# Kernel optimization log

Measured on AMD Instinct MI355X. Metric: run time of the kernel, lower is better.

## Reference

```python
import math
import jax, jax.numpy as jnp
import numpy as np

B = 128          # batch_size (graphs)
SEQ = 128        # max_seq_len (nodes per graph)
D = 128          # input_dim
HID = 64         # enc_hidden_dim
HEADS = 4        # in_head
N = B * SEQ      # total nodes
E = 262144       # edges (avg degree 16)


def _make_pe(seq, d):
    pos = np.arange(seq, dtype=np.float32)[:, None]
    i_even = np.arange(0, d, 2, dtype=np.float32)
    pe = np.zeros((seq, d), dtype=np.float32)
    pe[:, 0::2] = np.sin(pos / 10000.0 ** (2.0 * i_even / d))
    pe[:, 1::2] = np.cos(pos / 10000.0 ** (2.0 * (i_even + 1.0) / d))
    return jnp.asarray(pe)


def setup_inputs() -> dict:
    key = jax.random.key(0)
    ks = jax.random.split(key, 10)
    s = 0.1
    return {
        "x": jax.random.normal(ks[0], (N, D), jnp.float32),
        "edge_index": jax.random.randint(ks[1], (2, E), 0, N),
        "pe": _make_pe(SEQ, D),
        "W1": jax.random.normal(ks[2], (D, HEADS * HID), jnp.float32) * s,
        "a_src1": jax.random.normal(ks[3], (HEADS, HID), jnp.float32) * s,
        "a_dst1": jax.random.normal(ks[4], (HEADS, HID), jnp.float32) * s,
        "b1": jnp.zeros((HEADS * HID,), jnp.float32),
        "W2": jax.random.normal(ks[5], (HEADS * HID, HID), jnp.float32) * s,
        "a_src2": jax.random.normal(ks[6], (1, HID), jnp.float32) * s,
        "a_dst2": jax.random.normal(ks[7], (1, HID), jnp.float32) * s,
        "b2": jnp.zeros((HID,), jnp.float32),
        "batch_size": B,
    }


def _gat_conv(x, src, dst, W, a_src, a_dst, b, heads, ch, concat, n):
    # PyG GATConv (eval mode, self-loops already appended to src/dst).
    h = (x @ W).reshape(n, heads, ch)                      # [N,H,C]
    alpha_src = jnp.einsum("nhc,hc->nh", h, a_src)         # [N,H]
    alpha_dst = jnp.einsum("nhc,hc->nh", h, a_dst)
    e = jax.nn.leaky_relu(alpha_src[src] + alpha_dst[dst], 0.2)  # [E,H]
    m = jax.ops.segment_max(e, dst, num_segments=n)        # segment softmax over dst
    ex = jnp.exp(e - m[dst])
    den = jax.ops.segment_sum(ex, dst, num_segments=n)
    alpha = ex / (den[dst] + 1e-16)                        # [E,H]
    out = jax.ops.segment_sum(h[src] * alpha[:, :, None], dst, num_segments=n)
    out = out.reshape(n, heads * ch) if concat else out.mean(axis=1)
    return out + b


def reference(x, edge_index, pe, W1, a_src1, a_dst1, b1, W2, a_src2, a_dst2, b2, batch_size):
    n = x.shape[0]
    loop = jnp.arange(n)
    src = jnp.concatenate([edge_index[0], loop])           # add self-loops (PyG default)
    dst = jnp.concatenate([edge_index[1], loop])
    # positional encoding (dropout inactive in eval)
    h = x * math.sqrt(x.shape[1]) + jnp.tile(pe, (batch_size, 1))
    h = jax.nn.elu(_gat_conv(h, src, dst, W1, a_src1, a_dst1, b1, HEADS, HID, True, n))
    out = _gat_conv(h, src, dst, W2, a_src2, a_dst2, b2, 1, HID, False, n)
    return out.reshape(batch_size, -1, out.shape[1])
```

## Files before the change

### kernel.cpp

```cpp
#include <hip/hip_runtime.h>
#include <hip/hip_bf16.h>

typedef __hip_bfloat16 bf16;

#define N_NODES 16384
#define D_IN    128
#define HID     64
#define HEADS   4
#define F1      256
#define SEQ     128
#define SLOTS   64

__device__ __forceinline__ float wave_sum(float v) {
    #pragma unroll
    for (int o = 32; o > 0; o >>= 1) v += __shfl_xor(v, o, 64);
    return v;
}
__device__ __forceinline__ float lrelu(float v) { return v > 0.f ? v : 0.2f * v; }
__device__ __forceinline__ float rdlane(float v, int l) {
    return __uint_as_float(__builtin_amdgcn_readlane(__float_as_uint(v), l));
}

#define UNPACK8(u, te, acc)                                          \
    do {                                                             \
        acc[0] += (te) * __uint_as_float((u).x << 16);               \
        acc[1] += (te) * __uint_as_float((u).x & 0xffff0000u);       \
        acc[2] += (te) * __uint_as_float((u).y << 16);               \
        acc[3] += (te) * __uint_as_float((u).y & 0xffff0000u);       \
        acc[4] += (te) * __uint_as_float((u).z << 16);               \
        acc[5] += (te) * __uint_as_float((u).z & 0xffff0000u);       \
        acc[6] += (te) * __uint_as_float((u).w << 16);               \
        acc[7] += (te) * __uint_as_float((u).w & 0xffff0000u);       \
    } while (0)

__global__ __launch_bounds__(256) void k_gemm1z(const float* __restrict__ x,
                                                const float* __restrict__ pe,
                                                const float* __restrict__ W1,
                                                const float* __restrict__ a_src1,
                                                const float* __restrict__ a_dst1,
                                                bf16* __restrict__ h,
                                                float* __restrict__ as1,
                                                float* __restrict__ ad1,
                                                int4* __restrict__ cntv) {
    int tid = threadIdx.x, lane = tid & 63, wv = tid >> 6;
    if (tid < 4) cntv[blockIdx.x * 4 + tid] = make_int4(0, 0, 0, 0);

    int base = blockIdx.x * 16;
    int j4 = lane * 4;
    float2 xr[4];
    #pragma unroll
    for (int i = 0; i < 4; i++) {
        int row = base + wv * 4 + i;
        float2 xa  = *(const float2*)(x  + (size_t)row * 128 + 2 * lane);
        float2 pea = *(const float2*)(pe + (size_t)(row & (SEQ - 1)) * 128 + 2 * lane);
        xr[i].x = xa.x * 11.313708499f + pea.x;
        xr[i].y = xa.y * 11.313708499f + pea.y;
    }
    float acc[4][4] = {};
    const float4* Wv = (const float4*)W1;
    #pragma unroll 4
    for (int k2 = 0; k2 < 64; k2++) {
        float4 w0 = Wv[(size_t)(2 * k2) * 64 + lane];
        float4 w1 = Wv[(size_t)(2 * k2 + 1) * 64 + lane];
        #pragma unroll
        for (int i = 0; i < 4; i++) {
            float a0 = rdlane(xr[i].x, k2);
            float a1 = rdlane(xr[i].y, k2);
            acc[i][0] += a0 * w0.x + a1 * w1.x;
            acc[i][1] += a0 * w0.y + a1 * w1.y;
            acc[i][2] += a0 * w0.z + a1 * w1.z;
            acc[i][3] += a0 * w0.w + a1 * w1.w;
        }
    }
    float4 asv = *(const float4*)(a_src1 + j4);
    float4 adv = *(const float4*)(a_dst1 + j4);
    #pragma unroll
    for (int i = 0; i < 4; i++) {
        int row = base + wv * 4 + i;
        union { bf16 b[4]; ushort4 u; } cv;
        cv.b[0] = __float2bfloat16(acc[i][0]);
        cv.b[1] = __float2bfloat16(acc[i][1]);
        cv.b[2] = __float2bfloat16(acc[i][2]);
        cv.b[3] = __float2bfloat16(acc[i][3]);
        *(ushort4*)(h + (size_t)row * 256 + j4) = cv.u;
        float vs = acc[i][0] * asv.x + acc[i][1] * asv.y + acc[i][2] * asv.z + acc[i][3] * asv.w;
        float vd = acc[i][0] * adv.x + acc[i][1] * adv.y + acc[i][2] * adv.z + acc[i][3] * adv.w;
        #pragma unroll
        for (int o = 1; o < 16; o <<= 1) {
            vs += __shfl_xor(vs, o);
            vd += __shfl_xor(vd, o);
        }
        if ((lane & 15) == 0) {
            as1[row * 4 + (lane >> 4)] = vs;
            ad1[row * 4 + (lane >> 4)] = vd;
        }
    }
}

__global__ __launch_bounds__(256) void k_scatter(const int* __restrict__ ei, int E, int Etot,
                                                 int* __restrict__ cnt,
                                                 int* __restrict__ esrc,
                                                 const float* __restrict__ as1,
                                                 const float* __restrict__ ad1,
                                                 float* __restrict__ et) {
    int e = blockIdx.x * 256 + threadIdx.x;
    if (e >= Etot) return;
    int s, d;
    if (e < E) { s = ei[e]; d = ei[E + e]; }
    else       { s = e - E; d = s; }
    int pos = atomicAdd(&cnt[d], 1);
    if (pos < SLOTS) {
        esrc[d * SLOTS + pos] = s;
        float4 av = *(const float4*)(as1 + (size_t)s * 4);
        float4 bv = *(const float4*)(ad1 + (size_t)d * 4);
        size_t eb = (size_t)d * 4 * SLOTS + pos;
        et[eb + 0 * SLOTS] = __expf(lrelu(av.x + bv.x) - 40.f);
        et[eb + 1 * SLOTS] = __expf(lrelu(av.y + bv.y) - 40.f);
        et[eb + 2 * SLOTS] = __expf(lrelu(av.z + bv.z) - 40.f);
        et[eb + 3 * SLOTS] = __expf(lrelu(av.w + bv.w) - 40.f);
    }
}

__global__ __launch_bounds__(256) void k_agg1_gemm2(
        const int* __restrict__ cnt, const int* __restrict__ esrc,
        const float* __restrict__ et,
        const bf16* __restrict__ h,
        const float* __restrict__ b1,
        const float* __restrict__ W2,
        const float* __restrict__ a_src2, const float* __restrict__ a_dst2,
        bf16* __restrict__ h2, float* __restrict__ as2, float* __restrict__ ad2) {
    __shared__ float hs[8][256];
    __shared__ float part[4][8][64];
    int tid = threadIdx.x, lane = tid & 63, wv = tid >> 6;
    int dbase = blockIdx.x * 8;

    int eg = lane >> 3;
    int cg_ = lane & 7;
    const bf16* hbase = h + (size_t)wv * 64 + cg_ * 8;

    int cv = cnt[dbase + (lane & 7)];

    #pragma unroll 2
    for (int it = 0; it < 8; it++) {
        int d = dbase + it;
        int deg = min(__shfl(cv, it), SLOTS);
        int s = esrc[(size_t)d * SLOTS + lane] & (N_NODES - 1);
        float tv = et[((size_t)d * 4 + wv) * SLOTS + lane];
        float t = (lane < deg) ? tv : 0.f;

        float acc[8] = {0, 0, 0, 0, 0, 0, 0, 0};
        for (int sub = 0; sub < deg; sub += 32) {
            int qn = (min(deg - sub, 32) + 7) >> 3;
            int se0, se1, se2, se3; float te0, te1, te2, te3;
            uint4 u0, u1, u2, u3;
            se0 = __shfl(s, sub + eg);      te0 = __shfl(t, sub + eg);
            u0 = *(const uint4*)(hbase + (size_t)se0 * 256);
            if (qn > 1) {
                se1 = __shfl(s, sub + 8 + eg);  te1 = __shfl(t, sub + 8 + eg);
                u1 = *(const uint4*)(hbase + (size_t)se1 * 256);
            }
            if (qn > 2) {
                se2 = __shfl(s, sub + 16 + eg); te2 = __shfl(t, sub + 16 + eg);
                u2 = *(const uint4*)(hbase + (size_t)se2 * 256);
            }
            if (qn > 3) {
                se3 = __shfl(s, sub + 24 + eg); te3 = __shfl(t, sub + 24 + eg);
                u3 = *(const uint4*)(hbase + (size_t)se3 * 256);
            }
            UNPACK8(u0, te0, acc);
            if (qn > 1) UNPACK8(u1, te1, acc);
            if (qn > 2) UNPACK8(u2, te2, acc);
            if (qn > 3) UNPACK8(u3, te3, acc);
        }
        #pragma unroll
        for (int j = 0; j < 8; j++) {
            acc[j] += __shfl_xor(acc[j], 8);
            acc[j] += __shfl_xor(acc[j], 16);
            acc[j] += __shfl_xor(acc[j], 32);
        }
        float den = wave_sum(t);
        if (lane < 8) {
            float inv = 1.f / den;
            int cbase = wv * 64 + lane * 8;
            float o[8];
            #pragma unroll
            for (int j = 0; j < 8; j++) {
                float v = acc[j] * inv + b1[cbase + j];
                o[j] = v > 0.f ? v : (__expf(v) - 1.f);
            }
            float4* dst = (float4*)&hs[it][cbase];
            dst[0] = make_float4(o[0], o[1], o[2], o[3]);
            dst[1] = make_float4(o[4], o[5], o[6], o[7]);
        }
    }
    __syncthreads();

    {
        float acc2[8] = {0, 0, 0, 0, 0, 0, 0, 0};
        const int k4base = wv * 16;
        for (int kk = 0; kk < 16; kk++) {
            int k4 = k4base + kk;
            const float* wp = W2 + (size_t)k4 * 256 + lane;
            float w0 = wp[0], w1 = wp[64], w2 = wp[128], w3 = wp[192];
            #pragma unroll
            for (int r = 0; r < 8; r++) {
                float4 u = *(const float4*)&hs[r][k4 * 4];
                acc2[r] += u.x * w0 + u.y * w1 + u.z * w2 + u.w * w3;
            }
        }
        #pragma unroll
        for (int r = 0; r < 8; r++) part[wv][r][lane] = acc2[r];
    }
    __syncthreads();
    {
        int r0 = wv * 2, r1 = r0 + 1;
        float a0 = part[0][r0][lane] + part[1][r0][lane] + part[2][r0][lane] + part[3][r0][lane];
        float a1 = part[0][r1][lane] + part[1][r1][lane] + part[2][r1][lane] + part[3][r1][lane];
        float asj = a_src2[lane], adj = a_dst2[lane];
        int n0 = dbase + r0, n1 = dbase + r1;
        h2[(size_t)n0 * 64 + lane] = __float2bfloat16(a0);
        h2[(size_t)n1 * 64 + lane] = __float2bfloat16(a1);
        float va0 = wave_sum(a0 * asj);
        float vd0 = wave_sum(a0 * adj);
        float va1 = wave_sum(a1 * asj);
        float vd1 = wave_sum(a1 * adj);
        if (lane == 0) {
            as2[n0] = va0; ad2[n0] = vd0;
            as2[n1] = va1; ad2[n1] = vd1;
        }
    }
}

__global__ __launch_bounds__(256) void k_agg2(const int* __restrict__ cnt,
                                              const int* __restrict__ esrc,
                                              const bf16* __restrict__ h2,
                                              const float* __restrict__ as2,
                                              const float* __restrict__ ad2,
                                              const float* __restrict__ b2v,
                                              float* __restrict__ out) {
    int tid = threadIdx.x, lane = tid & 63, wv = tid >> 6;
    int d = blockIdx.x * 4 + wv;
    int deg = min(cnt[d], SLOTS);
    float adw = ad2[d];
    int eg = lane >> 3, cg_ = lane & 7;
    const bf16* hbase = h2 + cg_ * 8;

    int s = esrc[(size_t)d * SLOTS + lane] & (N_NODES - 1);
    float ev = as2[s];
    float t = (lane < deg) ? __expf(lrelu(ev + adw) - 40.f) : 0.f;

    float acc[8] = {0, 0, 0, 0, 0, 0, 0, 0};
    for (int sub = 0; sub < deg; sub += 32) {
        int qn = (min(deg - sub, 32) + 7) >> 3;
        int se0, se1, se2, se3; float te0, te1, te2, te3;
        uint4 u0, u1, u2, u3;
        se0 = __shfl(s, sub + eg);      te0 = __shfl(t, sub + eg);
        u0 = *(const uint4*)(hbase + (size_t)se0 * 64);
        if (qn > 1) {
            se1 = __shfl(s, sub + 8 + eg);  te1 = __shfl(t, sub + 8 + eg);
            u1 = *(const uint4*)(hbase + (size_t)se1 * 64);
        }
        if (qn > 2) {
            se2 = __shfl(s, sub + 16 + eg); te2 = __shfl(t, sub + 16 + eg);
            u2 = *(const uint4*)(hbase + (size_t)se2 * 64);
        }
        if (qn > 3) {
            se3 = __shfl(s, sub + 24 + eg); te3 = __shfl(t, sub + 24 + eg);
            u3 = *(const uint4*)(hbase + (size_t)se3 * 64);
        }
        UNPACK8(u0, te0, acc);
        if (qn > 1) UNPACK8(u1, te1, acc);
        if (qn > 2) UNPACK8(u2, te2, acc);
        if (qn > 3) UNPACK8(u3, te3, acc);
    }
    #pragma unroll
    for (int j = 0; j < 8; j++) {
        acc[j] += __shfl_xor(acc[j], 8);
        acc[j] += __shfl_xor(acc[j], 16);
        acc[j] += __shfl_xor(acc[j], 32);
    }
    float den = wave_sum(t);
    if (lane < 8) {
        float inv = 1.f / den;
        int cbase = lane * 8;
        float o[8];
        #pragma unroll
        for (int j = 0; j < 8; j++) o[j] = acc[j] * inv + b2v[cbase + j];
        float4* dst = (float4*)(out + (size_t)d * 64 + cbase);
        dst[0] = make_float4(o[0], o[1], o[2], o[3]);
        dst[1] = make_float4(o[4], o[5], o[6], o[7]);
    }
}

extern "C" void kernel_launch(void* const* d_in, const int* in_sizes, int n_in,
                              void* d_out, int out_size, void* d_ws, size_t ws_size,
                              hipStream_t stream) {
    const float* x    = (const float*)d_in[0];
    const int*   ei   = (const int*)  d_in[1];
    const float* pe   = (const float*)d_in[2];
    const float* W1   = (const float*)d_in[3];
    const float* a_s1 = (const float*)d_in[4];
    const float* a_d1 = (const float*)d_in[5];
    const float* b1   = (const float*)d_in[6];
    const float* W2   = (const float*)d_in[7];
    const float* a_s2 = (const float*)d_in[8];
    const float* a_d2 = (const float*)d_in[9];
    const float* b2   = (const float*)d_in[10];

    const int E    = in_sizes[1] / 2;
    const int n    = N_NODES;
    const int Etot = E + n;

    char* p = (char*)d_ws;
    auto alloc = [&](size_t bytes) -> void* {
        void* r = (void*)p;
        p += (bytes + 255) & ~(size_t)255;
        return r;
    };
    int*   cnt     = (int*)  alloc((size_t)n * 4);
    int*   esrc    = (int*)  alloc((size_t)n * SLOTS * 4);
    float* et      = (float*)alloc((size_t)n * HEADS * SLOTS * 4);
    bf16*  h       = (bf16*) alloc((size_t)n * F1 * 2);
    float* as1     = (float*)alloc((size_t)n * HEADS * 4);
    float* ad1     = (float*)alloc((size_t)n * HEADS * 4);
    bf16*  h2      = (bf16*) alloc((size_t)n * HID * 2);
    float* as2     = (float*)alloc((size_t)n * 4);
    float* ad2     = (float*)alloc((size_t)n * 4);

    int eblocks = (Etot + 255) / 256;

    k_gemm1z    <<<n / 16, 256, 0, stream>>>(x, pe, W1, a_s1, a_d1, h, as1, ad1, (int4*)cnt);
    k_scatter   <<<eblocks, 256, 0, stream>>>(ei, E, Etot, cnt, esrc, as1, ad1, et);
    k_agg1_gemm2<<<n / 8, 256, 0, stream>>>(cnt, esrc, et, h, b1,
                                            W2, a_s2, a_d2, h2, as2, ad2);
    k_agg2      <<<n / 4, 256, 0, stream>>>(cnt, esrc, h2, as2, ad2, b2, (float*)d_out);
}
```

Before: 183.5 us.

## Split edge-weight softmax into dedicated per-node kernels and pre-normalize attention

Edge attention logits are no longer computed inside the atomic scatter. Two new per-destination kernels compute them for both layers, normalize them by the wave-wide sum, and also zero unused slots of the slot table. The aggregation kernels then read source indices and normalized weights straight from memory instead of shuffling them and dividing by the denominator. This trades two extra launches and an extra pass over the edge arrays for a lighter scatter and simpler aggregation loops.

New measurement: 173.9 us. 5.2% less time.

```diff
diff --git a/kernel.cpp b/kernel.cpp
--- a/kernel.cpp
+++ b/kernel.cpp
@@ -99,26 +99,62 @@
 
 __global__ __launch_bounds__(256) void k_scatter(const int* __restrict__ ei, int E, int Etot,
                                                  int* __restrict__ cnt,
-                                                 int* __restrict__ esrc,
-                                                 const float* __restrict__ as1,
-                                                 const float* __restrict__ ad1,
-                                                 float* __restrict__ et) {
+                                                 int* __restrict__ esrc) {
     int e = blockIdx.x * 256 + threadIdx.x;
     if (e >= Etot) return;
     int s, d;
     if (e < E) { s = ei[e]; d = ei[E + e]; }
     else       { s = e - E; d = s; }
     int pos = atomicAdd(&cnt[d], 1);
-    if (pos < SLOTS) {
-        esrc[d * SLOTS + pos] = s;
+    if (pos < SLOTS) esrc[d * SLOTS + pos] = s;
+}
+
+__global__ __launch_bounds__(256) void k_edgew1(const int* __restrict__ cnt,
+                                                int* __restrict__ esrc,
+                                                const float* __restrict__ as1,
+                                                const float* __restrict__ ad1,
+                                                float* __restrict__ et) {
+    int tid = threadIdx.x, lane = tid & 63, wv = tid >> 6;
+    int d = blockIdx.x * 4 + wv;
+    int deg = min(cnt[d], SLOTS);
+    size_t rb = (size_t)d * SLOTS + lane;
+    int s = 0;
+    if (lane < deg) s = esrc[rb];
+    else            esrc[rb] = 0;
+    float4 bv = *(const float4*)(ad1 + (size_t)d * 4);
+    float t0 = 0.f, t1 = 0.f, t2 = 0.f, t3 = 0.f;
+    if (lane < deg) {
         float4 av = *(const float4*)(as1 + (size_t)s * 4);
-        float4 bv = *(const float4*)(ad1 + (size_t)d * 4);
-        size_t eb = (size_t)d * 4 * SLOTS + pos;
-        et[eb + 0 * SLOTS] = __expf(lrelu(av.x + bv.x) - 40.f);
-        et[eb + 1 * SLOTS] = __expf(lrelu(av.y + bv.y) - 40.f);
-        et[eb + 2 * SLOTS] = __expf(lrelu(av.z + bv.z) - 40.f);
-        et[eb + 3 * SLOTS] = __expf(lrelu(av.w + bv.w) - 40.f);
-    }
+        t0 = __expf(lrelu(av.x + bv.x) - 40.f);
+        t1 = __expf(lrelu(av.y + bv.y) - 40.f);
+        t2 = __expf(lrelu(av.z + bv.z) - 40.f);
+        t3 = __expf(lrelu(av.w + bv.w) - 40.f);
+    }
+    float i0 = 1.f / wave_sum(t0);
+    float i1 = 1.f / wave_sum(t1);
+    float i2 = 1.f / wave_sum(t2);
+    float i3 = 1.f / wave_sum(t3);
+    size_t eb = (size_t)d * 4 * SLOTS + lane;
+    et[eb + 0 * SLOTS] = t0 * i0;
+    et[eb + 1 * SLOTS] = t1 * i1;
+    et[eb + 2 * SLOTS] = t2 * i2;
+    et[eb + 3 * SLOTS] = t3 * i3;
+}
+
+__global__ __launch_bounds__(256) void k_edgew2(const int* __restrict__ cnt,
+                                                const int* __restrict__ esrc,
+                                                const float* __restrict__ as2,
+                                                const float* __restrict__ ad2,
+                                                float* __restrict__ et2) {
+    int tid = threadIdx.x, lane = tid & 63, wv = tid >> 6;
+    int d = blockIdx.x * 4 + wv;
+    int deg = min(cnt[d], SLOTS);
+    int s = esrc[(size_t)d * SLOTS + lane];
+    float ev = as2[s];
+    float adw = ad2[d];
+    float t = (lane < deg) ? __expf(lrelu(ev + adw) - 40.f) : 0.f;
+    float inv = 1.f / wave_sum(t);
+    et2[(size_t)d * SLOTS + lane] = t * inv;
 }
 
 __global__ __launch_bounds__(256) void k_agg1_gemm2(
@@ -138,33 +174,30 @@
     int cg_ = lane & 7;
     const bf16* hbase = h + (size_t)wv * 64 + cg_ * 8;
 
-    int cv = cnt[dbase + (lane & 7)];
-
     #pragma unroll 2
     for (int it = 0; it < 8; it++) {
         int d = dbase + it;
-        int deg = min(__shfl(cv, it), SLOTS);
-        int s = esrc[(size_t)d * SLOTS + lane] & (N_NODES - 1);
-        float tv = et[((size_t)d * 4 + wv) * SLOTS + lane];
-        float t = (lane < deg) ? tv : 0.f;
+        int deg = min(cnt[d], SLOTS);
+        const int*   ep = esrc + (size_t)d * SLOTS;
+        const float* tp = et + ((size_t)d * 4 + wv) * SLOTS;
 
         float acc[8] = {0, 0, 0, 0, 0, 0, 0, 0};
         for (int sub = 0; sub < deg; sub += 32) {
             int qn = (min(deg - sub, 32) + 7) >> 3;
             int se0, se1, se2, se3; float te0, te1, te2, te3;
             uint4 u0, u1, u2, u3;
-            se0 = __shfl(s, sub + eg);      te0 = __shfl(t, sub + eg);
+            se0 = ep[sub + eg];      te0 = tp[sub + eg];
             u0 = *(const uint4*)(hbase + (size_t)se0 * 256);
             if (qn > 1) {
-                se1 = __shfl(s, sub + 8 + eg);  te1 = __shfl(t, sub + 8 + eg);
+                se1 = ep[sub + 8 + eg];  te1 = tp[sub + 8 + eg];
                 u1 = *(const uint4*)(hbase + (size_t)se1 * 256);
             }
             if (qn > 2) {
-                se2 = __shfl(s, sub + 16 + eg); te2 = __shfl(t, sub + 16 + eg);
+                se2 = ep[sub + 16 + eg]; te2 = tp[sub + 16 + eg];
                 u2 = *(const uint4*)(hbase + (size_t)se2 * 256);
             }
             if (qn > 3) {
-                se3 = __shfl(s, sub + 24 + eg); te3 = __shfl(t, sub + 24 + eg);
+                se3 = ep[sub + 24 + eg]; te3 = tp[sub + 24 + eg];
                 u3 = *(const uint4*)(hbase + (size_t)se3 * 256);
             }
             UNPACK8(u0, te0, acc);
@@ -178,14 +211,12 @@
             acc[j] += __shfl_xor(acc[j], 16);
             acc[j] += __shfl_xor(acc[j], 32);
         }
-        float den = wave_sum(t);
         if (lane < 8) {
-            float inv = 1.f / den;
             int cbase = wv * 64 + lane * 8;
             float o[8];
             #pragma unroll
             for (int j = 0; j < 8; j++) {
-                float v = acc[j] * inv + b1[cbase + j];
+                float v = acc[j] + b1[cbase + j];
                 o[j] = v > 0.f ? v : (__expf(v) - 1.f);
             }
             float4* dst = (float4*)&hs[it][cbase];
@@ -233,39 +264,35 @@
 
 __global__ __launch_bounds__(256) void k_agg2(const int* __restrict__ cnt,
                                               const int* __restrict__ esrc,
+                                              const float* __restrict__ et2,
                                               const bf16* __restrict__ h2,
-                                              const float* __restrict__ as2,
-                                              const float* __restrict__ ad2,
                                               const float* __restrict__ b2v,
                                               float* __restrict__ out) {
     int tid = threadIdx.x, lane = tid & 63, wv = tid >> 6;
     int d = blockIdx.x * 4 + wv;
     int deg = min(cnt[d], SLOTS);
-    float adw = ad2[d];
     int eg = lane >> 3, cg_ = lane & 7;
     const bf16* hbase = h2 + cg_ * 8;
-
-    int s = esrc[(size_t)d * SLOTS + lane] & (N_NODES - 1);
-    float ev = as2[s];
-    float t = (lane < deg) ? __expf(lrelu(ev + adw) - 40.f) : 0.f;
+    const int*   ep = esrc + (size_t)d * SLOTS;
+    const float* tp = et2 + (size_t)d * SLOTS;
 
     float acc[8] = {0, 0, 0, 0, 0, 0, 0, 0};
     for (int sub = 0; sub < deg; sub += 32) {
         int qn = (min(deg - sub, 32) + 7) >> 3;
         int se0, se1, se2, se3; float te0, te1, te2, te3;
         uint4 u0, u1, u2, u3;
-        se0 = __shfl(s, sub + eg);      te0 = __shfl(t, sub + eg);
+        se0 = ep[sub + eg];      te0 = tp[sub + eg];
         u0 = *(const uint4*)(hbase + (size_t)se0 * 64);
         if (qn > 1) {
-            se1 = __shfl(s, sub + 8 + eg);  te1 = __shfl(t, sub + 8 + eg);
+            se1 = ep[sub + 8 + eg];  te1 = tp[sub + 8 + eg];
             u1 = *(const uint4*)(hbase + (size_t)se1 * 64);
         }
         if (qn > 2) {
-            se2 = __shfl(s, sub + 16 + eg); te2 = __shfl(t, sub + 16 + eg);
+            se2 = ep[sub + 16 + eg]; te2 = tp[sub + 16 + eg];
             u2 = *(const uint4*)(hbase + (size_t)se2 * 64);
         }
         if (qn > 3) {
-            se3 = __shfl(s, sub + 24 + eg); te3 = __shfl(t, sub + 24 + eg);
+            se3 = ep[sub + 24 + eg]; te3 = tp[sub + 24 + eg];
             u3 = *(const uint4*)(hbase + (size_t)se3 * 64);
         }
         UNPACK8(u0, te0, acc);
@@ -279,13 +306,11 @@
         acc[j] += __shfl_xor(acc[j], 16);
         acc[j] += __shfl_xor(acc[j], 32);
     }
-    float den = wave_sum(t);
     if (lane < 8) {
-        float inv = 1.f / den;
         int cbase = lane * 8;
         float o[8];
         #pragma unroll
-        for (int j = 0; j < 8; j++) o[j] = acc[j] * inv + b2v[cbase + j];
+        for (int j = 0; j < 8; j++) o[j] = acc[j] + b2v[cbase + j];
         float4* dst = (float4*)(out + (size_t)d * 64 + cbase);
         dst[0] = make_float4(o[0], o[1], o[2], o[3]);
         dst[1] = make_float4(o[4], o[5], o[6], o[7]);
@@ -326,12 +351,15 @@
     bf16*  h2      = (bf16*) alloc((size_t)n * HID * 2);
     float* as2     = (float*)alloc((size_t)n * 4);
     float* ad2     = (float*)alloc((size_t)n * 4);
+    float* et2     = et;
 
     int eblocks = (Etot + 255) / 256;
 
     k_gemm1z    <<<n / 16, 256, 0, stream>>>(x, pe, W1, a_s1, a_d1, h, as1, ad1, (int4*)cnt);
-    k_scatter   <<<eblocks, 256, 0, stream>>>(ei, E, Etot, cnt, esrc, as1, ad1, et);
+    k_scatter   <<<eblocks, 256, 0, stream>>>(ei, E, Etot, cnt, esrc);
+    k_edgew1    <<<n / 4, 256, 0, stream>>>(cnt, esrc, as1, ad1, et);
     k_agg1_gemm2<<<n / 8, 256, 0, stream>>>(cnt, esrc, et, h, b1,
                                             W2, a_s2, a_d2, h2, as2, ad2);
-    k_agg2      <<<n / 4, 256, 0, stream>>>(cnt, esrc, h2, as2, ad2, b2, (float*)d_out);
-}
+    k_edgew2    <<<n / 4, 256, 0, stream>>>(cnt, esrc, as2, ad2, et2);
+    k_agg2      <<<n / 4, 256, 0, stream>>>(cnt, esrc, et2, h2, b2, (float*)d_out);
+}
```
